# Kernel tuning notes

Measured on AMD Instinct MI355X. Metric: run time of the kernel, lower is better.

Reference implementation:

```python
import jax, jax.numpy as jnp
import numpy as np
import math

DIM = 768
MAX_STEP = 4
B, S = 32, 2048
LN_EPS = 1e-5
NORM_EPS = 1e-12


def _ln_relu(x, g, b):
    mu = jnp.mean(x, axis=-1, keepdims=True)
    var = jnp.mean((x - mu) ** 2, axis=-1, keepdims=True)
    return jax.nn.relu((x - mu) * jax.lax.rsqrt(var + LN_EPS) * g + b)


def _l2norm(v):  # torch F.normalize along dim=1
    n = jnp.sqrt(jnp.sum(v * v, axis=1, keepdims=True))
    return v / jnp.maximum(n, NORM_EPS)


def setup_inputs() -> dict:
    key = jax.random.key(0)
    ks = jax.random.split(key, 16)
    d = DIM
    inp = {
        "step": 0,
        "context": jax.random.normal(ks[0], (B, S, d), jnp.float32),
        "question": jax.random.normal(ks[1], (B, d), jnp.float32),
        "control": jax.random.normal(ks[2], (B, 2 * d), jnp.float32),
        "qm1": jax.random.randint(ks[3], (B, S), 0, 2).astype(jnp.float32),
        "qm2": jax.random.randint(ks[4], (B, S), 0, 2).astype(jnp.float32),
        "qm_l1": jax.random.randint(ks[5], (B,), 0, S).astype(jnp.int32),
        "qm_l2": jax.random.randint(ks[6], (B,), 0, S).astype(jnp.int32),
        # parameters (xavier-ish scale)
        "W_pos": jax.random.normal(ks[7], (MAX_STEP, d, d), jnp.float32) * (1.0 / math.sqrt(d)),
        "b_pos": jnp.zeros((MAX_STEP, d), jnp.float32),
        "ln1_g": jnp.ones((d,), jnp.float32), "ln1_b": jnp.zeros((d,), jnp.float32),
        "W_cq": jax.random.normal(ks[8], (3 * d, d), jnp.float32) * (1.0 / math.sqrt(3 * d)),
        "b_cq": jnp.zeros((d,), jnp.float32),
        "ln2_g": jnp.ones((d,), jnp.float32), "ln2_b": jnp.zeros((d,), jnp.float32),
        "W_attn": jax.random.normal(ks[9], (d, 1), jnp.float32) * (1.0 / math.sqrt(d)),
        "b_attn": jnp.zeros((1,), jnp.float32),
        "W_fuse": jax.random.normal(ks[10], (2 * d, d), jnp.float32) * (1.0 / math.sqrt(2 * d)),
        "b_fuse": jnp.zeros((d,), jnp.float32),
        "ln3_g": jnp.ones((d,), jnp.float32), "ln3_b": jnp.zeros((d,), jnp.float32),
        "ln4_g": jnp.ones((d,), jnp.float32), "ln4_b": jnp.zeros((d,), jnp.float32),
    }
    return inp


def reference(step, context, question, control, qm1, qm2, qm_l1, qm_l2,
              W_pos, b_pos, ln1_g, ln1_b, W_cq, b_cq, ln2_g, ln2_b,
              W_attn, b_attn, W_fuse, b_fuse, ln3_g, ln3_b, ln4_g, ln4_b):
    d = context.shape[-1]
    scale = 1.0 / math.sqrt(d)
    qm = qm1 + qm2  # [B,S]

    pa = _ln_relu(question @ W_pos[step] + b_pos[step], ln1_g, ln1_b)  # [B,d]
    cq = _ln_relu(jnp.concatenate([control, pa], axis=1) @ W_cq + b_cq, ln2_g, ln2_b)
    cqu = cq[:, None, :]  # [B,1,d]

    def scores(x, mask):  # x:[B,S,d], mask:[B,S]
        w = (x @ W_attn + b_attn) * scale  # [B,S,1] (dropout is identity in eval)
        w = jnp.where(mask[:, :, None] == 0, -1e9, w)
        return jax.nn.softmax(w, axis=1)

    attn = scores(cqu * context, qm)                     # [B,S,1]
    masked_ctx1 = context * qm1[:, :, None]
    masked_ctx2 = context * qm2[:, :, None]
    attn1 = scores(cqu * masked_ctx1, qm1)
    attn2 = scores(cqu * masked_ctx2, qm2)

    mc1 = _l2norm(jnp.sum(attn1 * masked_ctx1, axis=1))  # [B,d]
    mc2 = _l2norm(jnp.sum(attn2 * masked_ctx2, axis=1))
    ncf = _l2norm(jnp.sum(attn * context, axis=1))

    ctrl1 = _ln_relu(jnp.concatenate([mc1, ncf], axis=1) @ W_fuse + b_fuse, ln3_g, ln3_b)
    ctrl2 = _ln_relu(jnp.concatenate([mc2, ncf], axis=1) @ W_fuse + b_fuse, ln4_g, ln4_b)

    next_control = jnp.concatenate([ctrl1, ctrl2], axis=1)  # [B,2d]
    attentions = jnp.concatenate([attn[:, None], attn1[:, None], attn2[:, None]], axis=1)  # [B,3,S,1]
    return next_control, attentions
```

## Files before the change

### kernel.cpp

```cpp
#include <hip/hip_runtime.h>
#include <hip/hip_bf16.h>
#include <math.h>

#define DIM   768
#define BATCH 32
#define SEQ   2048
#define SCALE 0.036084391824351615f

__device__ __forceinline__ float wave_sum(float v) {
#pragma unroll
    for (int o = 32; o > 0; o >>= 1) v += __shfl_xor(v, o, 64);
    return v;
}

__device__ __forceinline__ void fma4(float4& a, float s, const float4& c) {
    a.x += s * c.x; a.y += s * c.y; a.z += s * c.z; a.w += s * c.w;
}

__global__ __launch_bounds__(256) void gemm_partial(
        const float* __restrict__ A0, int lda0,
        const float* __restrict__ A1, int lda1, int ksplit,
        const float* __restrict__ W,
        float* __restrict__ part, int Mtot,
        const int* __restrict__ step_ptr, int wstride) {
    const float* Wp = W + (step_ptr ? (long)step_ptr[0] * wstride : 0);
    const int jt = blockIdx.x * 64;
    const int r0 = blockIdx.y * 32;
    const int kc = blockIdx.z;
    __shared__ float As[32][33];
    __shared__ float Ws[32][64];
    const int t = threadIdx.x;
    const int j = t & 63;
    const int bg = t >> 6;
    float acc[8];
#pragma unroll
    for (int i = 0; i < 8; i++) acc[i] = 0.f;

    for (int k0 = kc * 64; k0 < kc * 64 + 64; k0 += 32) {
        {
            int r  = t >> 3;
            int kk = (t & 7) * 4;
            int ka = k0 + kk;
            float4 av;
            if (ka < ksplit)
                av = *(const float4*)(A0 + (long)(r0 + r) * lda0 + ka);
            else
                av = *(const float4*)(A1 + (long)(r0 + r) * lda1 + (ka - ksplit));
            As[r][kk] = av.x; As[r][kk + 1] = av.y; As[r][kk + 2] = av.z; As[r][kk + 3] = av.w;
        }
#pragma unroll
        for (int i = 0; i < 2; i++) {
            int idx = t + i * 256;
            int row = idx >> 4, col4 = idx & 15;
            float4 wv = *(const float4*)(Wp + (long)(k0 + row) * DIM + jt + col4 * 4);
            *(float4*)&Ws[row][col4 * 4] = wv;
        }
        __syncthreads();
#pragma unroll 8
        for (int kk = 0; kk < 32; kk++) {
            float wv = Ws[kk][j];
#pragma unroll
            for (int i = 0; i < 8; i++) acc[i] += As[bg * 8 + i][kk] * wv;
        }
        __syncthreads();
    }
#pragma unroll
    for (int i = 0; i < 8; i++)
        part[((long)(kc * Mtot + r0 + bg * 8 + i)) * DIM + jt + j] = acc[i];
}

__global__ __launch_bounds__(256) void reduce_ln(
        const float* __restrict__ part, int KC, int Mtot,
        const float* __restrict__ bias,
        const int* __restrict__ step_ptr, int bstride,
        const float* __restrict__ g, const float* __restrict__ b,
        const float* __restrict__ wattn,
        float* __restrict__ out) {
    const int row = blockIdx.x;
    const int t = threadIdx.x;
    const float* bp = bias + (step_ptr ? (long)step_ptr[0] * bstride : 0);
    __shared__ float r1[4], r2[4];
    float x[3];
    float s = 0.f, ss = 0.f;
#pragma unroll
    for (int i = 0; i < 3; i++) {
        int jj = t + i * 256;
        float v = bp[jj];
#pragma unroll 4
        for (int kc = 0; kc < KC; kc++)
            v += part[((long)(kc * Mtot + row)) * DIM + jj];
        x[i] = v; s += v; ss += v * v;
    }
    float wsv = wave_sum(s), wss = wave_sum(ss);
    int lane = t & 63, wid = t >> 6;
    if (lane == 0) { r1[wid] = wsv; r2[wid] = wss; }
    __syncthreads();
    s  = r1[0] + r1[1] + r1[2] + r1[3];
    ss = r2[0] + r2[1] + r2[2] + r2[3];
    float mu = s * (1.f / DIM);
    float var = ss * (1.f / DIM) - mu * mu;
    float rs = rsqrtf(var + 1e-5f);
#pragma unroll
    for (int i = 0; i < 3; i++) {
        int jj = t + i * 256;
        float y = (x[i] - mu) * rs * g[jj] + b[jj];
        y = y > 0.f ? y : 0.f;
        if (wattn) y *= wattn[jj];
        out[(long)row * DIM + jj] = y;
    }
}

__global__ __launch_bounds__(256) void reduce_ln_final(
        const float* __restrict__ part, int KC,
        const float* __restrict__ bias,
        const float* __restrict__ g3, const float* __restrict__ b3,
        const float* __restrict__ g4, const float* __restrict__ b4,
        float* __restrict__ nc) {
    const int row = blockIdx.x;
    const int t = threadIdx.x;
    __shared__ float r1[4], r2[4];
    float x[3];
    float s = 0.f, ss = 0.f;
#pragma unroll
    for (int i = 0; i < 3; i++) {
        int jj = t + i * 256;
        float v = bias[jj];
#pragma unroll 4
        for (int kc = 0; kc < KC; kc++)
            v += part[((long)(kc * 64 + row)) * DIM + jj];
        x[i] = v; s += v; ss += v * v;
    }
    float wsv = wave_sum(s), wss = wave_sum(ss);
    int lane = t & 63, wid = t >> 6;
    if (lane == 0) { r1[wid] = wsv; r2[wid] = wss; }
    __syncthreads();
    s  = r1[0] + r1[1] + r1[2] + r1[3];
    ss = r2[0] + r2[1] + r2[2] + r2[3];
    float mu = s * (1.f / DIM);
    float var = ss * (1.f / DIM) - mu * mu;
    float rs = rsqrtf(var + 1e-5f);
    const float* g  = (row < 32) ? g3 : g4;
    const float* bb = (row < 32) ? b3 : b4;
    int bidx = row & 31;
    int off  = (row < 32) ? 0 : DIM;
#pragma unroll
    for (int i = 0; i < 3; i++) {
        int jj = t + i * 256;
        float y = (x[i] - mu) * rs * g[jj] + bb[jj];
        nc[(long)bidx * (2 * DIM) + off + jj] = y > 0.f ? y : 0.f;
    }
}

__global__ __launch_bounds__(256) void attn_main(
        const float* __restrict__ ctx, const float* __restrict__ u,
        const float* __restrict__ b_attn,
        const float* __restrict__ qm1, const float* __restrict__ qm2,
        float* __restrict__ w, float* __restrict__ zpart,
        float* __restrict__ pvec) {
    const int c = blockIdx.x;
    const int b = blockIdx.y;
    const int t = threadIdx.x;
    const int wave = t >> 6, lane = t & 63;
    __shared__ float4 us4[192];
    __shared__ float4 red[4][3][192];
    if (t < 192) us4[t] = ((const float4*)(u + (long)b * DIM))[t];
    __syncthreads();
    const float batt = b_attn[0];
    const long row0 = (long)b * SEQ + c * 64;

    float4 acc[3][3];
#pragma unroll
    for (int k = 0; k < 3; k++)
#pragma unroll
        for (int i = 0; i < 3; i++) acc[k][i] = make_float4(0.f, 0.f, 0.f, 0.f);
    float zacc[3] = {0.f, 0.f, 0.f};

#pragma unroll 1
    for (int g = 0; g < 4; g++) {
        const int rw = g * 16 + wave * 4;
        float4 cr[4][3];
        float d[4];
#pragma unroll
        for (int rr = 0; rr < 4; rr++) {
            const float4* crow = (const float4*)(ctx + (row0 + rw + rr) * DIM);
            float dd = 0.f;
#pragma unroll
            for (int i = 0; i < 3; i++) {
                float4 cv = crow[lane + i * 64];
                cr[rr][i] = cv;
                float4 uu = us4[lane + i * 64];
                dd += cv.x * uu.x + cv.y * uu.y + cv.z * uu.z + cv.w * uu.w;
            }
            d[rr] = wave_sum(dd);
        }
        float lw0 = (d[0] + batt) * SCALE;
        float lw1 = (d[1] + batt) * SCALE;
        float lw2 = (d[2] + batt) * SCALE;
        float lw3 = (d[3] + batt) * SCALE;
        if (lane < 4) {
            float v = lane == 0 ? lw0 : lane == 1 ? lw1 : lane == 2 ? lw2 : lw3;
            w[row0 + rw + lane] = v;
        }
        float mv = 0.f;
        if (lane < 4) mv = qm1[row0 + rw + lane];
        else if (lane < 8) mv = qm2[row0 + rw + lane - 4];
#pragma unroll
        for (int rr = 0; rr < 4; rr++) {
            float a1 = __shfl(mv, rr, 64);
            float a2 = __shfl(mv, rr + 4, 64);
            float lwr = rr == 0 ? lw0 : rr == 1 ? lw1 : rr == 2 ? lw2 : lw3;
            float ev = __expf(lwr);
            float e0 = (a1 != 0.f || a2 != 0.f) ? ev : 0.f;
            float e1 = (a1 != 0.f) ? ev : 0.f;
            float e2 = (a2 != 0.f) ? ev : 0.f;
            zacc[0] += e0; zacc[1] += e1; zacc[2] += e2;
#pragma unroll
            for (int i = 0; i < 3; i++) {
                fma4(acc[0][i], e0, cr[rr][i]);
                fma4(acc[1][i], e1, cr[rr][i]);
                fma4(acc[2][i], e2, cr[rr][i]);
            }
        }
    }
    if (lane == 0) {
        float* zp = zpart + ((long)(b * 32 + c) * 4 + wave) * 3;
        zp[0] = zacc[0]; zp[1] = zacc[1]; zp[2] = zacc[2];
    }
#pragma unroll
    for (int k = 0; k < 3; k++)
#pragma unroll
        for (int i = 0; i < 3; i++)
            red[wave][k][lane + i * 64] = acc[k][i];
    __syncthreads();
    for (int idx = t; idx < 576; idx += 256) {
        int k = idx / 192, col = idx - k * 192;
        float4 a = red[0][k][col], bb = red[1][k][col];
        float4 cc = red[2][k][col], dd = red[3][k][col];
        float4 s;
        s.x = a.x + bb.x + cc.x + dd.x;
        s.y = a.y + bb.y + cc.y + dd.y;
        s.z = a.z + bb.z + cc.z + dd.z;
        s.w = a.w + bb.w + cc.w + dd.w;
        ((float4*)pvec)[((long)(b * 32 + c) * 3 + k) * 192 + col] = s;
    }
}

__global__ __launch_bounds__(256) void combine_norm(
        const float* __restrict__ zpart, const float* __restrict__ pvec,
        const float* __restrict__ w,
        const float* __restrict__ qm1, const float* __restrict__ qm2,
        float* __restrict__ A6, float* __restrict__ attn_out) {
    const int b = blockIdx.x, k = blockIdx.y;
    const int t = threadIdx.x;
    const int lane = t & 63, wid = t >> 6;
    __shared__ float r1[4], r2[4];
    float z = 0.f;
    for (int j = t; j < 128; j += 256)
        z += zpart[((long)(b * 32 + (j >> 2)) * 4 + (j & 3)) * 3 + k];
    z = wave_sum(z);
    if (lane == 0) r1[wid] = z;
    __syncthreads();
    z = r1[0] + r1[1] + r1[2] + r1[3];
    float v[3] = {0.f, 0.f, 0.f};
    for (int cch = 0; cch < 32; cch++) {
        const float* p = pvec + ((long)(b * 32 + cch) * 3 + k) * DIM;
#pragma unroll
        for (int i = 0; i < 3; i++) v[i] += p[t + i * 256];
    }
    float ss = v[0] * v[0] + v[1] * v[1] + v[2] * v[2];
    float wss = wave_sum(ss);
    if (lane == 0) r2[wid] = wss;
    __syncthreads();
    ss = r2[0] + r2[1] + r2[2] + r2[3];
    float inv = 1.f / fmaxf(sqrtf(ss), 1e-12f);
#pragma unroll
    for (int i = 0; i < 3; i++) {
        int jj = t + i * 256;
        float nv = v[i] * inv;
        if (k == 0) {
            A6[(long)b * (2 * DIM) + DIM + jj] = nv;
            A6[(long)(32 + b) * (2 * DIM) + DIM + jj] = nv;
        } else if (k == 1) {
            A6[(long)b * (2 * DIM) + jj] = nv;
        } else {
            A6[(long)(32 + b) * (2 * DIM) + jj] = nv;
        }
    }
    float iz = 1.f / z;
#pragma unroll
    for (int ii = 0; ii < 8; ii++) {
        int s = t + ii * 256;
        float wv = w[(long)b * SEQ + s];
        float m1 = qm1[(long)b * SEQ + s];
        float m2 = qm2[(long)b * SEQ + s];
        bool act = (k == 0) ? (m1 != 0.f || m2 != 0.f) : (k == 1) ? (m1 != 0.f) : (m2 != 0.f);
        attn_out[((long)b * 3 + k) * SEQ + s] = act ? __expf(wv) * iz : 0.f;
    }
}

extern "C" void kernel_launch(void* const* d_in, const int* in_sizes, int n_in,
                              void* d_out, int out_size, void* d_ws, size_t ws_size,
                              hipStream_t stream) {
    const int*   step     = (const int*)  d_in[0];
    const float* ctx      = (const float*)d_in[1];
    const float* question = (const float*)d_in[2];
    const float* control  = (const float*)d_in[3];
    const float* qm1      = (const float*)d_in[4];
    const float* qm2      = (const float*)d_in[5];
    const float* W_pos    = (const float*)d_in[8];
    const float* b_pos    = (const float*)d_in[9];
    const float* ln1_g    = (const float*)d_in[10];
    const float* ln1_b    = (const float*)d_in[11];
    const float* W_cq     = (const float*)d_in[12];
    const float* b_cq     = (const float*)d_in[13];
    const float* ln2_g    = (const float*)d_in[14];
    const float* ln2_b    = (const float*)d_in[15];
    const float* W_attn   = (const float*)d_in[16];
    const float* b_attn   = (const float*)d_in[17];
    const float* W_fuse   = (const float*)d_in[18];
    const float* b_fuse   = (const float*)d_in[19];
    const float* ln3_g    = (const float*)d_in[20];
    const float* ln3_b    = (const float*)d_in[21];
    const float* ln4_g    = (const float*)d_in[22];
    const float* ln4_b    = (const float*)d_in[23];

    float* ws    = (float*)d_ws;
    float* pa    = ws;
    float* u     = ws + 24576;
    float* w     = ws + 49152;
    float* zpart = ws + 114688;
    float* A6    = ws + 126976;
    float* big   = ws + 225280;

    float* nc_out   = (float*)d_out;
    float* attn_out = (float*)d_out + BATCH * 2 * DIM;

    gemm_partial<<<dim3(DIM / 64, 1, DIM / 64), 256, 0, stream>>>(
        question, DIM, question, DIM, 1 << 30, W_pos, big, 32, step, DIM * DIM);
    reduce_ln<<<BATCH, 256, 0, stream>>>(big, DIM / 64, 32, b_pos, step, DIM,
                                         ln1_g, ln1_b, nullptr, pa);

    gemm_partial<<<dim3(DIM / 64, 1, (3 * DIM) / 64), 256, 0, stream>>>(
        control, 2 * DIM, pa, DIM, 2 * DIM, W_cq, big, 32, nullptr, 0);
    reduce_ln<<<BATCH, 256, 0, stream>>>(big, (3 * DIM) / 64, 32, b_cq, nullptr, 0,
                                         ln2_g, ln2_b, W_attn, u);

    attn_main<<<dim3(SEQ / 64, BATCH), 256, 0, stream>>>(
        ctx, u, b_attn, qm1, qm2, w, zpart, big);

    combine_norm<<<dim3(BATCH, 3), 256, 0, stream>>>(
        zpart, big, w, qm1, qm2, A6, attn_out);

    gemm_partial<<<dim3(DIM / 64, 2, (2 * DIM) / 64), 256, 0, stream>>>(
        A6, 2 * DIM, A6, 2 * DIM, 1 << 30, W_fuse, big, 64, nullptr, 0);
    reduce_ln_final<<<2 * BATCH, 256, 0, stream>>>(big, (2 * DIM) / 64, b_fuse,
                                                   ln3_g, ln3_b, ln4_g, ln4_b, nc_out);
}
```

Baseline: 98.11 us.

## Software-pipeline context row loads in attn_main with register double buffering

Each wave now owns a contiguous block of 16 rows and processes them two at a time. The next pair of context rows is prefetched into a second register buffer while the current pair is reduced and accumulated. The u vector is held in registers instead of shared memory, which drops the initial __syncthreads. The mask values for all 16 rows are loaded once up front rather than once per group. This should hide global-load latency in a bandwidth-bound pass, at the cost of higher register pressure from the double buffer and full unrolling.

```diff
diff --git a/kernel.cpp b/kernel.cpp
--- a/kernel.cpp
+++ b/kernel.cpp
@@ -161,12 +161,17 @@
     const int b = blockIdx.y;
     const int t = threadIdx.x;
     const int wave = t >> 6, lane = t & 63;
-    __shared__ float4 us4[192];
     __shared__ float4 red[4][3][192];
-    if (t < 192) us4[t] = ((const float4*)(u + (long)b * DIM))[t];
-    __syncthreads();
     const float batt = b_attn[0];
-    const long row0 = (long)b * SEQ + c * 64;
+    const long row0 = (long)b * SEQ + c * 64 + wave * 16;
+
+    float4 uu[3];
+#pragma unroll
+    for (int i = 0; i < 3; i++)
+        uu[i] = ((const float4*)(u + (long)b * DIM))[lane + i * 64];
+    float mv = 0.f;
+    if (lane < 16) mv = qm1[row0 + lane];
+    else if (lane >= 32 && lane < 48) mv = qm2[row0 + lane - 32];
 
     float4 acc[3][3];
 #pragma unroll
@@ -175,40 +180,42 @@
         for (int i = 0; i < 3; i++) acc[k][i] = make_float4(0.f, 0.f, 0.f, 0.f);
     float zacc[3] = {0.f, 0.f, 0.f};
 
-#pragma unroll 1
-    for (int g = 0; g < 4; g++) {
-        const int rw = g * 16 + wave * 4;
-        float4 cr[4][3];
-        float d[4];
-#pragma unroll
-        for (int rr = 0; rr < 4; rr++) {
-            const float4* crow = (const float4*)(ctx + (row0 + rw + rr) * DIM);
-            float dd = 0.f;
-#pragma unroll
-            for (int i = 0; i < 3; i++) {
-                float4 cv = crow[lane + i * 64];
-                cr[rr][i] = cv;
-                float4 uu = us4[lane + i * 64];
-                dd += cv.x * uu.x + cv.y * uu.y + cv.z * uu.z + cv.w * uu.w;
+    float4 crA[2][3], crB[2][3];
+#pragma unroll
+    for (int rr = 0; rr < 2; rr++) {
+        const float4* p = (const float4*)(ctx + (row0 + rr) * DIM);
+#pragma unroll
+        for (int i = 0; i < 3; i++) crA[rr][i] = p[lane + i * 64];
+    }
+#pragma unroll
+    for (int g = 0; g < 8; g++) {
+        float4 (&cur)[2][3] = (g & 1) ? crB : crA;
+        float4 (&nxt)[2][3] = (g & 1) ? crA : crB;
+        if (g < 7) {
+#pragma unroll
+            for (int rr = 0; rr < 2; rr++) {
+                const float4* p = (const float4*)(ctx + (row0 + (g + 1) * 2 + rr) * DIM);
+#pragma unroll
+                for (int i = 0; i < 3; i++) nxt[rr][i] = p[lane + i * 64];
             }
-            d[rr] = wave_sum(dd);
-        }
-        float lw0 = (d[0] + batt) * SCALE;
-        float lw1 = (d[1] + batt) * SCALE;
-        float lw2 = (d[2] + batt) * SCALE;
-        float lw3 = (d[3] + batt) * SCALE;
-        if (lane < 4) {
-            float v = lane == 0 ? lw0 : lane == 1 ? lw1 : lane == 2 ? lw2 : lw3;
-            w[row0 + rw + lane] = v;
-        }
-        float mv = 0.f;
-        if (lane < 4) mv = qm1[row0 + rw + lane];
-        else if (lane < 8) mv = qm2[row0 + rw + lane - 4];
-#pragma unroll
-        for (int rr = 0; rr < 4; rr++) {
-            float a1 = __shfl(mv, rr, 64);
-            float a2 = __shfl(mv, rr + 4, 64);
-            float lwr = rr == 0 ? lw0 : rr == 1 ? lw1 : rr == 2 ? lw2 : lw3;
+        }
+        float d0 = 0.f, d1 = 0.f;
+#pragma unroll
+        for (int i = 0; i < 3; i++) {
+            d0 += cur[0][i].x * uu[i].x + cur[0][i].y * uu[i].y
+                + cur[0][i].z * uu[i].z + cur[0][i].w * uu[i].w;
+            d1 += cur[1][i].x * uu[i].x + cur[1][i].y * uu[i].y
+                + cur[1][i].z * uu[i].z + cur[1][i].w * uu[i].w;
+        }
+        d0 = wave_sum(d0); d1 = wave_sum(d1);
+        float lw0 = (d0 + batt) * SCALE;
+        float lw1 = (d1 + batt) * SCALE;
+        if (lane < 2) w[row0 + g * 2 + lane] = lane ? lw1 : lw0;
+#pragma unroll
+        for (int rr = 0; rr < 2; rr++) {
+            float lwr = rr ? lw1 : lw0;
+            float a1 = __shfl(mv, g * 2 + rr, 64);
+            float a2 = __shfl(mv, 32 + g * 2 + rr, 64);
             float ev = __expf(lwr);
             float e0 = (a1 != 0.f || a2 != 0.f) ? ev : 0.f;
             float e1 = (a1 != 0.f) ? ev : 0.f;
@@ -216,9 +223,9 @@
             zacc[0] += e0; zacc[1] += e1; zacc[2] += e2;
 #pragma unroll
             for (int i = 0; i < 3; i++) {
-                fma4(acc[0][i], e0, cr[rr][i]);
-                fma4(acc[1][i], e1, cr[rr][i]);
-                fma4(acc[2][i], e2, cr[rr][i]);
+                fma4(acc[0][i], e0, cur[rr][i]);
+                fma4(acc[1][i], e1, cur[rr][i]);
+                fma4(acc[2][i], e2, cur[rr][i]);
             }
         }
     }
@@ -234,13 +241,13 @@
     __syncthreads();
     for (int idx = t; idx < 576; idx += 256) {
         int k = idx / 192, col = idx - k * 192;
-        float4 a = red[0][k][col], bb = red[1][k][col];
-        float4 cc = red[2][k][col], dd = red[3][k][col];
+        float4 a = red[0][k][col], b2 = red[1][k][col];
+        float4 c2 = red[2][k][col], d2 = red[3][k][col];
         float4 s;
-        s.x = a.x + bb.x + cc.x + dd.x;
-        s.y = a.y + bb.y + cc.y + dd.y;
-        s.z = a.z + bb.z + cc.z + dd.z;
-        s.w = a.w + bb.w + cc.w + dd.w;
+        s.x = a.x + b2.x + c2.x + d2.x;
+        s.y = a.y + b2.y + c2.y + d2.y;
+        s.z = a.z + b2.z + c2.z + d2.z;
+        s.w = a.w + b2.w + c2.w + d2.w;
         ((float4*)pvec)[((long)(b * 32 + c) * 3 + k) * 192 + col] = s;
     }
 }
```

After: 104.4 us. 1.06x slower.

## Fuse small GEMM/LN stages into persistent kernels with atomic-counter grid sync

Applied to the files above, without the earlier changes.

Collapses the eight launches into three kernels plus a memset. Pre- and post-stages now chain their partial GEMM and LayerNorm steps through global atomic counters and spin-waits, and the last attention block per batch does the combine/normalise step. This removes launch gaps and tail bubbles between tiny kernels. It relies on all 432 or 576 blocks being co-resident to avoid deadlock in the spin-waits, and it adds an extra memset launch.

```diff
diff --git a/kernel.cpp b/kernel.cpp
--- a/kernel.cpp
+++ b/kernel.cpp
@@ -17,16 +17,23 @@
     a.x += s * c.x; a.y += s * c.y; a.z += s * c.z; a.w += s * c.w;
 }
 
-__global__ __launch_bounds__(256) void gemm_partial(
+__device__ __forceinline__ void spin_wait(int* c, int target) {
+    if (threadIdx.x == 0) {
+        while (atomicAdd(c, 0) < target) __builtin_amdgcn_s_sleep(2);
+        __threadfence();
+    }
+    __syncthreads();
+}
+__device__ __forceinline__ void signal_done(int* c) {
+    __syncthreads();
+    if (threadIdx.x == 0) { __threadfence(); atomicAdd(c, 1); }
+}
+
+__device__ __forceinline__ void gemm_tile(
         const float* __restrict__ A0, int lda0,
         const float* __restrict__ A1, int lda1, int ksplit,
-        const float* __restrict__ W,
-        float* __restrict__ part, int Mtot,
-        const int* __restrict__ step_ptr, int wstride) {
-    const float* Wp = W + (step_ptr ? (long)step_ptr[0] * wstride : 0);
-    const int jt = blockIdx.x * 64;
-    const int r0 = blockIdx.y * 32;
-    const int kc = blockIdx.z;
+        const float* __restrict__ Wp,
+        float* __restrict__ part, int Mtot, int r0, int jt, int kc) {
     __shared__ float As[32][33];
     __shared__ float Ws[32][64];
     const int t = threadIdx.x;
@@ -69,16 +76,13 @@
         part[((long)(kc * Mtot + r0 + bg * 8 + i)) * DIM + jt + j] = acc[i];
 }
 
-__global__ __launch_bounds__(256) void reduce_ln(
+__device__ __forceinline__ void ln_row(
         const float* __restrict__ part, int KC, int Mtot,
-        const float* __restrict__ bias,
-        const int* __restrict__ step_ptr, int bstride,
+        const float* __restrict__ bp,
         const float* __restrict__ g, const float* __restrict__ b,
         const float* __restrict__ wattn,
-        float* __restrict__ out) {
-    const int row = blockIdx.x;
+        float* __restrict__ out, int row) {
     const int t = threadIdx.x;
-    const float* bp = bias + (step_ptr ? (long)step_ptr[0] * bstride : 0);
     __shared__ float r1[4], r2[4];
     float x[3];
     float s = 0.f, ss = 0.f;
@@ -86,7 +90,6 @@
     for (int i = 0; i < 3; i++) {
         int jj = t + i * 256;
         float v = bp[jj];
-#pragma unroll 4
         for (int kc = 0; kc < KC; kc++)
             v += part[((long)(kc * Mtot + row)) * DIM + jj];
         x[i] = v; s += v; ss += v * v;
@@ -108,46 +111,41 @@
         if (wattn) y *= wattn[jj];
         out[(long)row * DIM + jj] = y;
     }
-}
-
-__global__ __launch_bounds__(256) void reduce_ln_final(
-        const float* __restrict__ part, int KC,
-        const float* __restrict__ bias,
-        const float* __restrict__ g3, const float* __restrict__ b3,
-        const float* __restrict__ g4, const float* __restrict__ b4,
-        float* __restrict__ nc) {
-    const int row = blockIdx.x;
-    const int t = threadIdx.x;
-    __shared__ float r1[4], r2[4];
-    float x[3];
-    float s = 0.f, ss = 0.f;
-#pragma unroll
-    for (int i = 0; i < 3; i++) {
-        int jj = t + i * 256;
-        float v = bias[jj];
-#pragma unroll 4
-        for (int kc = 0; kc < KC; kc++)
-            v += part[((long)(kc * 64 + row)) * DIM + jj];
-        x[i] = v; s += v; ss += v * v;
-    }
-    float wsv = wave_sum(s), wss = wave_sum(ss);
-    int lane = t & 63, wid = t >> 6;
-    if (lane == 0) { r1[wid] = wsv; r2[wid] = wss; }
-    __syncthreads();
-    s  = r1[0] + r1[1] + r1[2] + r1[3];
-    ss = r2[0] + r2[1] + r2[2] + r2[3];
-    float mu = s * (1.f / DIM);
-    float var = ss * (1.f / DIM) - mu * mu;
-    float rs = rsqrtf(var + 1e-5f);
-    const float* g  = (row < 32) ? g3 : g4;
-    const float* bb = (row < 32) ? b3 : b4;
-    int bidx = row & 31;
-    int off  = (row < 32) ? 0 : DIM;
-#pragma unroll
-    for (int i = 0; i < 3; i++) {
-        int jj = t + i * 256;
-        float y = (x[i] - mu) * rs * g[jj] + bb[jj];
-        nc[(long)bidx * (2 * DIM) + off + jj] = y > 0.f ? y : 0.f;
+    __syncthreads();
+}
+
+__global__ __launch_bounds__(256, 4) void pre_kernel(
+        const float* __restrict__ question, const float* __restrict__ control,
+        const float* __restrict__ W_pos, const float* __restrict__ b_pos,
+        const int* __restrict__ step_ptr,
+        const float* __restrict__ ln1_g, const float* __restrict__ ln1_b,
+        const float* __restrict__ W_cq, const float* __restrict__ b_cq,
+        const float* __restrict__ ln2_g, const float* __restrict__ ln2_b,
+        const float* __restrict__ W_attn,
+        float* __restrict__ part1, float* __restrict__ pa,
+        float* __restrict__ part2, float* __restrict__ u,
+        int* __restrict__ cnt) {
+    const int i = blockIdx.x;
+    const int st = step_ptr[0];
+    int* c1 = cnt + 0; int* c2 = cnt + 1; int* c3 = cnt + 2;
+
+    if (i < 144) {
+        gemm_tile(question, DIM, question, DIM, 1 << 30,
+                  W_pos + (long)st * DIM * DIM, part1, 32, 0, (i % 12) * 64, i / 12);
+        signal_done(c1);
+    }
+    if (i < 32) {
+        spin_wait(c1, 144);
+        ln_row(part1, 12, 32, b_pos + (long)st * DIM, ln1_g, ln1_b, nullptr, pa, i);
+        signal_done(c2);
+    }
+    spin_wait(c2, 32);
+    gemm_tile(control, 2 * DIM, pa, DIM, 2 * DIM, W_cq, part2, 32, 0,
+              (i % 12) * 64, i / 12);
+    signal_done(c3);
+    if (i < 32) {
+        spin_wait(c3, 432);
+        ln_row(part2, 36, 32, b_cq, ln2_g, ln2_b, W_attn, u, i);
     }
 }
 
@@ -156,7 +154,8 @@
         const float* __restrict__ b_attn,
         const float* __restrict__ qm1, const float* __restrict__ qm2,
         float* __restrict__ w, float* __restrict__ zpart,
-        float* __restrict__ pvec) {
+        float* __restrict__ pvec, int* __restrict__ cnt_b,
+        float* __restrict__ A6, float* __restrict__ attn_out) {
     const int c = blockIdx.x;
     const int b = blockIdx.y;
     const int t = threadIdx.x;
@@ -234,67 +233,120 @@
     __syncthreads();
     for (int idx = t; idx < 576; idx += 256) {
         int k = idx / 192, col = idx - k * 192;
-        float4 a = red[0][k][col], bb = red[1][k][col];
-        float4 cc = red[2][k][col], dd = red[3][k][col];
+        float4 a = red[0][k][col], b2 = red[1][k][col];
+        float4 c2 = red[2][k][col], d2 = red[3][k][col];
         float4 s;
-        s.x = a.x + bb.x + cc.x + dd.x;
-        s.y = a.y + bb.y + cc.y + dd.y;
-        s.z = a.z + bb.z + cc.z + dd.z;
-        s.w = a.w + bb.w + cc.w + dd.w;
+        s.x = a.x + b2.x + c2.x + d2.x;
+        s.y = a.y + b2.y + c2.y + d2.y;
+        s.z = a.z + b2.z + c2.z + d2.z;
+        s.w = a.w + b2.w + c2.w + d2.w;
         ((float4*)pvec)[((long)(b * 32 + c) * 3 + k) * 192 + col] = s;
     }
-}
-
-__global__ __launch_bounds__(256) void combine_norm(
-        const float* __restrict__ zpart, const float* __restrict__ pvec,
-        const float* __restrict__ w,
-        const float* __restrict__ qm1, const float* __restrict__ qm2,
-        float* __restrict__ A6, float* __restrict__ attn_out) {
-    const int b = blockIdx.x, k = blockIdx.y;
+
+    __shared__ int lastflag;
+    __syncthreads();
+    if (t == 0) {
+        __threadfence();
+        int old = atomicAdd(&cnt_b[b], 1);
+        lastflag = (old == 31);
+        if (old == 31) __threadfence();
+    }
+    __syncthreads();
+    if (!lastflag) return;
+
+    __shared__ float zr[4], sr[4];
+#pragma unroll 1
+    for (int k = 0; k < 3; k++) {
+        float z = 0.f;
+        if (t < 128) z = zpart[((long)(b * 32 + (t >> 2)) * 4 + (t & 3)) * 3 + k];
+        z = wave_sum(z);
+        if (lane == 0) zr[wave] = z;
+        float v0 = 0.f, v1 = 0.f, v2 = 0.f;
+        for (int cch = 0; cch < 32; cch++) {
+            const float* p = pvec + ((long)(b * 32 + cch) * 3 + k) * DIM;
+            v0 += p[t]; v1 += p[t + 256]; v2 += p[t + 512];
+        }
+        float ss = v0 * v0 + v1 * v1 + v2 * v2;
+        float wss = wave_sum(ss);
+        if (lane == 0) sr[wave] = wss;
+        __syncthreads();
+        float zz = zr[0] + zr[1] + zr[2] + zr[3];
+        float sst = sr[0] + sr[1] + sr[2] + sr[3];
+        float inv = 1.f / fmaxf(sqrtf(sst), 1e-12f);
+        float vv[3] = {v0, v1, v2};
+#pragma unroll
+        for (int ii = 0; ii < 3; ii++) {
+            int jj = t + ii * 256;
+            float nv = vv[ii] * inv;
+            if (k == 0) {
+                A6[(long)b * (2 * DIM) + DIM + jj] = nv;
+                A6[(long)(32 + b) * (2 * DIM) + DIM + jj] = nv;
+            } else if (k == 1) {
+                A6[(long)b * (2 * DIM) + jj] = nv;
+            } else {
+                A6[(long)(32 + b) * (2 * DIM) + jj] = nv;
+            }
+        }
+        float iz = 1.f / zz;
+#pragma unroll
+        for (int ii = 0; ii < 8; ii++) {
+            int s = t + ii * 256;
+            float wv = w[(long)b * SEQ + s];
+            float m1 = qm1[(long)b * SEQ + s];
+            float m2 = qm2[(long)b * SEQ + s];
+            bool act = (k == 0) ? (m1 != 0.f || m2 != 0.f)
+                     : (k == 1) ? (m1 != 0.f) : (m2 != 0.f);
+            attn_out[((long)b * 3 + k) * SEQ + s] = act ? __expf(wv) * iz : 0.f;
+        }
+        __syncthreads();
+    }
+}
+
+__global__ __launch_bounds__(256, 4) void post_kernel(
+        const float* __restrict__ A6, const float* __restrict__ W_fuse,
+        float* __restrict__ part3, const float* __restrict__ b_fuse,
+        const float* __restrict__ ln3_g, const float* __restrict__ ln3_b,
+        const float* __restrict__ ln4_g, const float* __restrict__ ln4_b,
+        float* __restrict__ nc, int* __restrict__ cnt) {
+    const int i = blockIdx.x;
     const int t = threadIdx.x;
-    const int lane = t & 63, wid = t >> 6;
-    __shared__ float r1[4], r2[4];
-    float z = 0.f;
-    for (int j = t; j < 128; j += 256)
-        z += zpart[((long)(b * 32 + (j >> 2)) * 4 + (j & 3)) * 3 + k];
-    z = wave_sum(z);
-    if (lane == 0) r1[wid] = z;
-    __syncthreads();
-    z = r1[0] + r1[1] + r1[2] + r1[3];
-    float v[3] = {0.f, 0.f, 0.f};
-    for (int cch = 0; cch < 32; cch++) {
-        const float* p = pvec + ((long)(b * 32 + cch) * 3 + k) * DIM;
-#pragma unroll
-        for (int i = 0; i < 3; i++) v[i] += p[t + i * 256];
-    }
-    float ss = v[0] * v[0] + v[1] * v[1] + v[2] * v[2];
-    float wss = wave_sum(ss);
-    if (lane == 0) r2[wid] = wss;
-    __syncthreads();
-    ss = r2[0] + r2[1] + r2[2] + r2[3];
-    float inv = 1.f / fmaxf(sqrtf(ss), 1e-12f);
-#pragma unroll
-    for (int i = 0; i < 3; i++) {
-        int jj = t + i * 256;
-        float nv = v[i] * inv;
-        if (k == 0) {
-            A6[(long)b * (2 * DIM) + DIM + jj] = nv;
-            A6[(long)(32 + b) * (2 * DIM) + DIM + jj] = nv;
-        } else if (k == 1) {
-            A6[(long)b * (2 * DIM) + jj] = nv;
-        } else {
-            A6[(long)(32 + b) * (2 * DIM) + jj] = nv;
-        }
-    }
-    float iz = 1.f / z;
-#pragma unroll
-    for (int ii = 0; ii < 8; ii++) {
-        int s = t + ii * 256;
-        float wv = w[(long)b * SEQ + s];
-        float m1 = qm1[(long)b * SEQ + s];
-        float m2 = qm2[(long)b * SEQ + s];
-        bool act = (k == 0) ? (m1 != 0.f || m2 != 0.f) : (k == 1) ? (m1 != 0.f) : (m2 != 0.f);
-        attn_out[((long)b * 3 + k) * SEQ + s] = act ? __expf(wv) * iz : 0.f;
+    int* c4 = cnt + 3;
+    gemm_tile(A6, 2 * DIM, A6, 2 * DIM, 1 << 30, W_fuse, part3, 64,
+              ((i / 12) % 2) * 32, (i % 12) * 64, i / 24);
+    signal_done(c4);
+    if (i < 64) {
+        spin_wait(c4, 576);
+        const int row = i;
+        __shared__ float r1[4], r2[4];
+        float x[3];
+        float s = 0.f, ss = 0.f;
+#pragma unroll
+        for (int ii = 0; ii < 3; ii++) {
+            int jj = t + ii * 256;
+            float v = b_fuse[jj];
+            for (int kc = 0; kc < 24; kc++)
+                v += part3[((long)(kc * 64 + row)) * DIM + jj];
+            x[ii] = v; s += v; ss += v * v;
+        }
+        float wsv = wave_sum(s), wss = wave_sum(ss);
+        int lane = t & 63, wid = t >> 6;
+        if (lane == 0) { r1[wid] = wsv; r2[wid] = wss; }
+        __syncthreads();
+        s  = r1[0] + r1[1] + r1[2] + r1[3];
+        ss = r2[0] + r2[1] + r2[2] + r2[3];
+        float mu = s * (1.f / DIM);
+        float var = ss * (1.f / DIM) - mu * mu;
+        float rs = rsqrtf(var + 1e-5f);
+        const float* g  = (row < 32) ? ln3_g : ln4_g;
+        const float* bb = (row < 32) ? ln3_b : ln4_b;
+        int bidx = row & 31;
+        int off  = (row < 32) ? 0 : DIM;
+#pragma unroll
+        for (int ii = 0; ii < 3; ii++) {
+            int jj = t + ii * 256;
+            float y = (x[ii] - mu) * rs * g[jj] + bb[jj];
+            nc[(long)bidx * (2 * DIM) + off + jj] = y > 0.f ? y : 0.f;
+        }
     }
 }
 
@@ -324,35 +376,30 @@
     const float* ln4_g    = (const float*)d_in[22];
     const float* ln4_b    = (const float*)d_in[23];
 
-    float* ws    = (float*)d_ws;
-    float* pa    = ws;
-    float* u     = ws + 24576;
-    float* w     = ws + 49152;
-    float* zpart = ws + 114688;
-    float* A6    = ws + 126976;
-    float* big   = ws + 225280;
+    int*   cnt  = (int*)d_ws;
+    float* base = (float*)d_ws + 64;
+    float* pa    = base;
+    float* u     = base + 24576;
+    float* w     = base + 49152;
+    float* zpart = base + 114688;
+    float* A6    = base + 126976;
+    float* part1 = base + 225280;
+    float* part2 = base + 520192;
+    float* part3 = base + 1404928;
+    float* pvec  = base + 2584576;
 
     float* nc_out   = (float*)d_out;
     float* attn_out = (float*)d_out + BATCH * 2 * DIM;
 
-    gemm_partial<<<dim3(DIM / 64, 1, DIM / 64), 256, 0, stream>>>(
-        question, DIM, question, DIM, 1 << 30, W_pos, big, 32, step, DIM * DIM);
-    reduce_ln<<<BATCH, 256, 0, stream>>>(big, DIM / 64, 32, b_pos, step, DIM,
-                                         ln1_g, ln1_b, nullptr, pa);
-
-    gemm_partial<<<dim3(DIM / 64, 1, (3 * DIM) / 64), 256, 0, stream>>>(
-        control, 2 * DIM, pa, DIM, 2 * DIM, W_cq, big, 32, nullptr, 0);
-    reduce_ln<<<BATCH, 256, 0, stream>>>(big, (3 * DIM) / 64, 32, b_cq, nullptr, 0,
-                                         ln2_g, ln2_b, W_attn, u);
+    hipMemsetAsync(d_ws, 0, 256, stream);
+
+    pre_kernel<<<432, 256, 0, stream>>>(
+        question, control, W_pos, b_pos, step, ln1_g, ln1_b,
+        W_cq, b_cq, ln2_g, ln2_b, W_attn, part1, pa, part2, u, cnt);
 
     attn_main<<<dim3(SEQ / 64, BATCH), 256, 0, stream>>>(
-        ctx, u, b_attn, qm1, qm2, w, zpart, big);
-
-    combine_norm<<<dim3(BATCH, 3), 256, 0, stream>>>(
-        zpart, big, w, qm1, qm2, A6, attn_out);
-
-    gemm_partial<<<dim3(DIM / 64, 2, (2 * DIM) / 64), 256, 0, stream>>>(
-        A6, 2 * DIM, A6, 2 * DIM, 1 << 30, W_fuse, big, 64, nullptr, 0);
-    reduce_ln_final<<<2 * BATCH, 256, 0, stream>>>(big, (2 * DIM) / 64, b_fuse,
-                                                   ln3_g, ln3_b, ln4_g, ln4_b, nc_out);
-}
+        ctx, u, b_attn, qm1, qm2, w, zpart, pvec, cnt + 8, A6, attn_out);
+
+    post_kernel<<<576, 256, 0, stream>>>(
+        A6, W_fuse, part3, b_fuse, ln3_g, ln3_b, ln4_g, ln4_b, nc_out, cnt);
+}
```

New measurement: 196.6 us. 100% more time.

## Cut attn_main LDS footprint and raise occupancy with serialized wave reduction

Applied to the files above, without the earlier changes.

The attention kernel now keeps the u vector in registers instead of shared memory. It replaces the 4-wave shared reduction buffer with a single buffer that the waves accumulate into one after another, which shrinks LDS per block from about 39KB to about 9KB. It also adds a launch-bounds hint for four blocks per CU. The goal is more resident blocks to hide memory latency on the streaming context read, at the cost of extra barriers and a serialized reduction step.

```diff
diff --git a/kernel.cpp b/kernel.cpp
--- a/kernel.cpp
+++ b/kernel.cpp
@@ -151,7 +151,7 @@
     }
 }
 
-__global__ __launch_bounds__(256) void attn_main(
+__global__ __launch_bounds__(256, 4) void attn_main(
         const float* __restrict__ ctx, const float* __restrict__ u,
         const float* __restrict__ b_attn,
         const float* __restrict__ qm1, const float* __restrict__ qm2,
@@ -161,12 +161,14 @@
     const int b = blockIdx.y;
     const int t = threadIdx.x;
     const int wave = t >> 6, lane = t & 63;
-    __shared__ float4 us4[192];
-    __shared__ float4 red[4][3][192];
-    if (t < 192) us4[t] = ((const float4*)(u + (long)b * DIM))[t];
-    __syncthreads();
+    __shared__ float4 red[3][192];
     const float batt = b_attn[0];
     const long row0 = (long)b * SEQ + c * 64;
+
+    float4 uu[3];
+#pragma unroll
+    for (int i = 0; i < 3; i++)
+        uu[i] = ((const float4*)(u + (long)b * DIM))[lane + i * 64];
 
     float4 acc[3][3];
 #pragma unroll
@@ -188,8 +190,7 @@
             for (int i = 0; i < 3; i++) {
                 float4 cv = crow[lane + i * 64];
                 cr[rr][i] = cv;
-                float4 uu = us4[lane + i * 64];
-                dd += cv.x * uu.x + cv.y * uu.y + cv.z * uu.z + cv.w * uu.w;
+                dd += cv.x * uu[i].x + cv.y * uu[i].y + cv.z * uu[i].z + cv.w * uu[i].w;
             }
             d[rr] = wave_sum(dd);
         }
@@ -226,22 +227,31 @@
         float* zp = zpart + ((long)(b * 32 + c) * 4 + wave) * 3;
         zp[0] = zacc[0]; zp[1] = zacc[1]; zp[2] = zacc[2];
     }
-#pragma unroll
-    for (int k = 0; k < 3; k++)
-#pragma unroll
-        for (int i = 0; i < 3; i++)
-            red[wave][k][lane + i * 64] = acc[k][i];
-    __syncthreads();
+    if (wave == 0) {
+#pragma unroll
+        for (int k = 0; k < 3; k++)
+#pragma unroll
+            for (int i = 0; i < 3; i++) red[k][lane + i * 64] = acc[k][i];
+    }
+    __syncthreads();
+#pragma unroll 1
+    for (int wv = 1; wv < 4; wv++) {
+        if (wave == wv) {
+#pragma unroll
+            for (int k = 0; k < 3; k++)
+#pragma unroll
+                for (int i = 0; i < 3; i++) {
+                    float4 r = red[k][lane + i * 64];
+                    r.x += acc[k][i].x; r.y += acc[k][i].y;
+                    r.z += acc[k][i].z; r.w += acc[k][i].w;
+                    red[k][lane + i * 64] = r;
+                }
+        }
+        __syncthreads();
+    }
     for (int idx = t; idx < 576; idx += 256) {
         int k = idx / 192, col = idx - k * 192;
-        float4 a = red[0][k][col], bb = red[1][k][col];
-        float4 cc = red[2][k][col], dd = red[3][k][col];
-        float4 s;
-        s.x = a.x + bb.x + cc.x + dd.x;
-        s.y = a.y + bb.y + cc.y + dd.y;
-        s.z = a.z + bb.z + cc.z + dd.z;
-        s.w = a.w + bb.w + cc.w + dd.w;
-        ((float4*)pvec)[((long)(b * 32 + c) * 3 + k) * 192 + col] = s;
+        ((float4*)pvec)[((long)(b * 32 + c) * 3 + k) * 192 + col] = red[k][col];
     }
 }
 
```

After: 102.8 us. 4.8% more time.
